# Performance work log

Hardware: AMD Instinct MI355X
Metric: run time of the kernel (lower is better)

## Reference

```python
import jax, jax.numpy as jnp
import numpy as np

NUM_SEQS = 32
MAX_PREFILL = 512
TOTAL_TOKENS = NUM_SEQS * MAX_PREFILL  # 16384
D_MODEL = 4096
VOCAB = 50257


def setup_inputs() -> dict:
    key = jax.random.key(0)
    k1, k2, k3 = jax.random.split(key, 3)
    hidden_states = jax.random.normal(k1, (TOTAL_TOKENS, D_MODEL), dtype=jnp.float32)
    embd_weight = jax.random.normal(k2, (VOCAB, D_MODEL), dtype=jnp.float32) * 0.02
    # per-sequence prefill lengths in [1, MAX_PREFILL]; cumsum <= TOTAL_TOKENS
    prefill_lens = jax.random.randint(k3, (NUM_SEQS,), 1, MAX_PREFILL + 1, dtype=jnp.int32)
    return {"hidden_states": hidden_states, "embd_weight": embd_weight,
            "prefill_lens": prefill_lens}


def reference(hidden_states, embd_weight, prefill_lens):
    # last-token index of each sequence in the flattened token stream
    indices = jnp.cumsum(prefill_lens) - 1            # [num_seqs]
    last_h = hidden_states[indices]                   # [num_seqs, d_model]
    logits = jnp.matmul(last_h, embd_weight.T)        # [num_seqs, vocab]
    logprobs = jax.nn.log_softmax(logits.astype(jnp.float32), axis=-1)
    ids = jnp.argmax(logprobs, axis=-1)               # [num_seqs]
    return ids
```

## Files before the change

kernel.cpp:

```cpp
#include <hip/hip_runtime.h>
#include <hip/hip_bf16.h>

#define D_MODEL 4096
#define VOCAB 50257
#define NUM_SEQS 32
#define NT 1571

typedef __attribute__((ext_vector_type(8))) short bf16x8;
typedef __attribute__((ext_vector_type(16))) float f32x16;


__device__ __forceinline__ void cvt2(float f, short* hi, short* lo) {
  union { __hip_bfloat16 b; short s; } h, l;
  h.b = __float2bfloat16(f);
  float hf = __bfloat162float(h.b);
  l.b = __float2bfloat16(f - hf);
  *hi = h.s; *lo = l.s;
}

__global__ void k_prep(const int* __restrict__ lens, int* __restrict__ idx) {
  if (threadIdx.x == 0) {
    int run = 0;
    for (int s = 0; s < NUM_SEQS; ++s) { run += lens[s]; idx[s] = run - 1; }
  }
}

__global__ void k_gather(const float* __restrict__ hs, const int* __restrict__ idx,
                         short* __restrict__ hBh, short* __restrict__ hBl) {
  int g = blockIdx.x * 512 + threadIdx.x;
  int s = g >> 12, k = g & 4095;
  float v = hs[(size_t)idx[s] * D_MODEL + k];
  short hi, lo; cvt2(v, &hi, &lo);
  int off = ((k >> 3) * 32 + s) * 8 + (k & 7);
  hBh[off] = hi; hBl[off] = lo;
}

__global__ __launch_bounds__(64) void k_mfma(const float* __restrict__ W,
    const short* __restrict__ hBh, const short* __restrict__ hBl,
    unsigned long long* __restrict__ wbest) {
  const int lane = threadIdx.x;
  const int half = lane >> 5;
  const int r32 = lane & 31;
  const int tile = blockIdx.x;
  const int wrow = min(tile * 32 + r32, VOCAB - 1);
  const float* wp = W + (size_t)wrow * D_MODEL + half * 8;
  const short* bph = hBh + ((size_t)half * 32 + r32) * 8;
  const short* bpl = hBl + ((size_t)half * 32 + r32) * 8;

  f32x16 accA, accB;
#pragma unroll
  for (int i = 0; i < 16; ++i) { accA[i] = 0.f; accB[i] = 0.f; }

  float4 a0 = *(const float4*)(wp);
  float4 a1 = *(const float4*)(wp + 4);
  float4 p0 = *(const float4*)(wp + 16);
  float4 p1 = *(const float4*)(wp + 20);
  bf16x8 bh = *(const bf16x8*)(bph);
  bf16x8 bl = *(const bf16x8*)(bpl);

#pragma unroll 1
  for (int t = 0; t < 256; ++t) {
    const int t2 = (t + 2 < 256) ? t + 2 : 0;
    const int t1 = (t + 1 < 256) ? t + 1 : 0;
    float4 n0 = *(const float4*)(wp + 16 * t2);
    float4 n1 = *(const float4*)(wp + 16 * t2 + 4);
    bf16x8 nbh = *(const bf16x8*)(bph + 512 * t1);
    bf16x8 nbl = *(const bf16x8*)(bpl + 512 * t1);

    float fa[8] = {a0.x, a0.y, a0.z, a0.w, a1.x, a1.y, a1.z, a1.w};
    bf16x8 ahi, alo;
#pragma unroll
    for (int e = 0; e < 8; ++e) {
      short hi, lo; cvt2(fa[e], &hi, &lo);
      ahi[e] = hi; alo[e] = lo;
    }

    accA = __builtin_amdgcn_mfma_f32_32x32x16_bf16(ahi, bh, accA, 0, 0, 0);
    accB = __builtin_amdgcn_mfma_f32_32x32x16_bf16(ahi, bl, accB, 0, 0, 0);
    accA = __builtin_amdgcn_mfma_f32_32x32x16_bf16(alo, bh, accA, 0, 0, 0);

    a0 = p0; a1 = p1; p0 = n0; p1 = n1; bh = nbh; bl = nbl;
  }

#pragma unroll
  for (int i = 0; i < 16; ++i) accA[i] += accB[i];

  unsigned long long best = 0ull;
#pragma unroll
  for (int r = 0; r < 16; ++r) {
    int row = (r & 3) + 8 * (r >> 2) + 4 * half;
    int v = tile * 32 + row;
    if (v < VOCAB) {
      unsigned u = __float_as_uint(accA[r]);
      u = (u & 0x80000000u) ? ~u : (u | 0x80000000u);
      unsigned long long key = ((unsigned long long)u << 32) | (unsigned)(~v);
      if (key > best) best = key;
    }
  }
  unsigned long long o = __shfl_xor(best, 32, 64);
  if (o > best) best = o;
  if (half == 0) wbest[(size_t)tile * 32 + r32] = best;
}

__global__ __launch_bounds__(256) void k_final(
    const unsigned long long* __restrict__ wbest, int* __restrict__ out) {
  int s = blockIdx.x;
  unsigned long long best = 0ull;
  for (int i = threadIdx.x; i < NT; i += 256) {
    unsigned long long k = wbest[(size_t)i * 32 + s];
    if (k > best) best = k;
  }
#pragma unroll
  for (int off = 32; off > 0; off >>= 1) {
    unsigned long long o = __shfl_xor(best, off, 64);
    if (o > best) best = o;
  }
  __shared__ unsigned long long lred[4];
  if ((threadIdx.x & 63) == 0) lred[threadIdx.x >> 6] = best;
  __syncthreads();
  if (threadIdx.x == 0) {
#pragma unroll
    for (int i = 1; i < 4; ++i) if (lred[i] > best) best = lred[i];
    out[s] = (int)(~(unsigned)(best & 0xFFFFFFFFull));
  }
}

extern "C" void kernel_launch(void* const* d_in, const int* in_sizes, int n_in,
                              void* d_out, int out_size, void* d_ws, size_t ws_size,
                              hipStream_t stream) {
  const float* hs  = (const float*)d_in[0];
  const float* W   = (const float*)d_in[1];
  const int* lens  = (const int*)d_in[2];

  char* ws = (char*)d_ws;
  int* idx = (int*)ws;
  short* hBh = (short*)(ws + 4096);
  short* hBl = (short*)(ws + 266240);
  unsigned long long* wbest = (unsigned long long*)(ws + 528384);
  int* out = (int*)d_out;

  k_prep<<<1, 64, 0, stream>>>(lens, idx);
  k_gather<<<256, 512, 0, stream>>>(hs, idx, hBh, hBl);
  k_mfma<<<NT, 64, 0, stream>>>(W, hBh, hBl, wbest);
  k_final<<<NUM_SEQS, 256, 0, stream>>>(wbest, out);
}
```

Baseline: 204.5 us.

## Split K across two waves per tile, deepen prefetch, reduce argmax via atomicMax

Each 32-row vocab tile is now processed by two waves, each covering half of the K dimension, and their partial accumulators are combined through shared memory. The W prefetch depth goes from two to three steps. Per-tile best keys are merged with a 64-bit atomicMax into a 32-entry global array instead of a per-tile buffer and a reduction kernel, leaving k_final as a trivial decode. This raises memory-level parallelism for streaming the fp32 weight matrix, at the cost of an LDS exchange, a barrier and atomic contention on 32 addresses.

```diff
diff --git a/kernel.cpp b/kernel.cpp
--- a/kernel.cpp
+++ b/kernel.cpp
@@ -5,6 +5,8 @@
 #define VOCAB 50257
 #define NUM_SEQS 32
 #define NT 1571
+#define KW 2048
+#define TSTEPS (KW / 16)
 
 typedef __attribute__((ext_vector_type(8))) short bf16x8;
 typedef __attribute__((ext_vector_type(16))) float f32x16;
@@ -18,11 +20,14 @@
   *hi = h.s; *lo = l.s;
 }
 
-__global__ void k_prep(const int* __restrict__ lens, int* __restrict__ idx) {
-  if (threadIdx.x == 0) {
+__global__ void k_prep(const int* __restrict__ lens, int* __restrict__ idx,
+                       unsigned long long* __restrict__ gkeys) {
+  int t = threadIdx.x;
+  if (t == 0) {
     int run = 0;
     for (int s = 0; s < NUM_SEQS; ++s) { run += lens[s]; idx[s] = run - 1; }
   }
+  if (t < NUM_SEQS) gkeys[t] = 0ull;
 }
 
 __global__ void k_gather(const float* __restrict__ hs, const int* __restrict__ idx,
@@ -35,35 +40,35 @@
   hBh[off] = hi; hBl[off] = lo;
 }
 
-__global__ __launch_bounds__(64) void k_mfma(const float* __restrict__ W,
+__global__ __launch_bounds__(128) void k_mfma(const float* __restrict__ W,
     const short* __restrict__ hBh, const short* __restrict__ hBl,
-    unsigned long long* __restrict__ wbest) {
-  const int lane = threadIdx.x;
+    unsigned long long* __restrict__ gkeys) {
+  const int lane = threadIdx.x & 63;
+  const int wv = threadIdx.x >> 6;
   const int half = lane >> 5;
   const int r32 = lane & 31;
   const int tile = blockIdx.x;
   const int wrow = min(tile * 32 + r32, VOCAB - 1);
-  const float* wp = W + (size_t)wrow * D_MODEL + half * 8;
-  const short* bph = hBh + ((size_t)half * 32 + r32) * 8;
-  const short* bpl = hBl + ((size_t)half * 32 + r32) * 8;
+  const int k0 = wv * KW;
+  const float4* wr = (const float4*)(W + (size_t)wrow * D_MODEL + k0 + half * 8);
+  const short* bph = hBh + (((size_t)(k0 >> 3) + half) * 32 + r32) * 8;
+  const short* bpl = hBl + (((size_t)(k0 >> 3) + half) * 32 + r32) * 8;
 
   f32x16 accA, accB;
 #pragma unroll
   for (int i = 0; i < 16; ++i) { accA[i] = 0.f; accB[i] = 0.f; }
 
-  float4 a0 = *(const float4*)(wp);
-  float4 a1 = *(const float4*)(wp + 4);
-  float4 p0 = *(const float4*)(wp + 16);
-  float4 p1 = *(const float4*)(wp + 20);
+  float4 a0 = wr[0], a1 = wr[1];
+  float4 b0 = wr[4], b1 = wr[5];
+  float4 c0 = wr[8], c1 = wr[9];
   bf16x8 bh = *(const bf16x8*)(bph);
   bf16x8 bl = *(const bf16x8*)(bpl);
 
 #pragma unroll 1
-  for (int t = 0; t < 256; ++t) {
-    const int t2 = (t + 2 < 256) ? t + 2 : 0;
-    const int t1 = (t + 1 < 256) ? t + 1 : 0;
-    float4 n0 = *(const float4*)(wp + 16 * t2);
-    float4 n1 = *(const float4*)(wp + 16 * t2 + 4);
+  for (int t = 0; t < TSTEPS; ++t) {
+    const int t3 = (t + 3 < TSTEPS) ? t + 3 : 0;
+    const int t1 = (t + 1 < TSTEPS) ? t + 1 : 0;
+    float4 d0 = wr[4 * t3], d1 = wr[4 * t3 + 1];
     bf16x8 nbh = *(const bf16x8*)(bph + 512 * t1);
     bf16x8 nbl = *(const bf16x8*)(bpl + 512 * t1);
 
@@ -79,50 +84,46 @@
     accB = __builtin_amdgcn_mfma_f32_32x32x16_bf16(ahi, bl, accB, 0, 0, 0);
     accA = __builtin_amdgcn_mfma_f32_32x32x16_bf16(alo, bh, accA, 0, 0, 0);
 
-    a0 = p0; a1 = p1; p0 = n0; p1 = n1; bh = nbh; bl = nbl;
+    a0 = b0; a1 = b1; b0 = c0; b1 = c1; c0 = d0; c1 = d1;
+    bh = nbh; bl = nbl;
   }
 
 #pragma unroll
   for (int i = 0; i < 16; ++i) accA[i] += accB[i];
 
-  unsigned long long best = 0ull;
+  __shared__ float red[64][17];
+  if (wv == 1) {
 #pragma unroll
-  for (int r = 0; r < 16; ++r) {
-    int row = (r & 3) + 8 * (r >> 2) + 4 * half;
-    int v = tile * 32 + row;
-    if (v < VOCAB) {
-      unsigned u = __float_as_uint(accA[r]);
-      u = (u & 0x80000000u) ? ~u : (u | 0x80000000u);
-      unsigned long long key = ((unsigned long long)u << 32) | (unsigned)(~v);
-      if (key > best) best = key;
+    for (int i = 0; i < 16; ++i) red[lane][i] = accA[i];
+  }
+  __syncthreads();
+  if (wv == 0) {
+#pragma unroll
+    for (int i = 0; i < 16; ++i) accA[i] += red[lane][i];
+
+    unsigned long long best = 0ull;
+#pragma unroll
+    for (int r = 0; r < 16; ++r) {
+      int row = (r & 3) + 8 * (r >> 2) + 4 * half;
+      int v = tile * 32 + row;
+      if (v < VOCAB) {
+        unsigned u = __float_as_uint(accA[r]);
+        u = (u & 0x80000000u) ? ~u : (u | 0x80000000u);
+        unsigned long long key = ((unsigned long long)u << 32) | (unsigned)(~v);
+        if (key > best) best = key;
+      }
     }
+    unsigned long long o = __shfl_xor(best, 32, 64);
+    if (o > best) best = o;
+    if (half == 0) atomicMax(&gkeys[r32], best);
   }
-  unsigned long long o = __shfl_xor(best, 32, 64);
-  if (o > best) best = o;
-  if (half == 0) wbest[(size_t)tile * 32 + r32] = best;
 }
 
-__global__ __launch_bounds__(256) void k_final(
-    const unsigned long long* __restrict__ wbest, int* __restrict__ out) {
-  int s = blockIdx.x;
-  unsigned long long best = 0ull;
-  for (int i = threadIdx.x; i < NT; i += 256) {
-    unsigned long long k = wbest[(size_t)i * 32 + s];
-    if (k > best) best = k;
-  }
-#pragma unroll
-  for (int off = 32; off > 0; off >>= 1) {
-    unsigned long long o = __shfl_xor(best, off, 64);
-    if (o > best) best = o;
-  }
-  __shared__ unsigned long long lred[4];
-  if ((threadIdx.x & 63) == 0) lred[threadIdx.x >> 6] = best;
-  __syncthreads();
-  if (threadIdx.x == 0) {
-#pragma unroll
-    for (int i = 1; i < 4; ++i) if (lred[i] > best) best = lred[i];
-    out[s] = (int)(~(unsigned)(best & 0xFFFFFFFFull));
-  }
+__global__ void k_final(const unsigned long long* __restrict__ gkeys,
+                        int* __restrict__ out) {
+  int s = threadIdx.x;
+  if (s < NUM_SEQS)
+    out[s] = (int)(~(unsigned)(gkeys[s] & 0xFFFFFFFFull));
 }
 
 extern "C" void kernel_launch(void* const* d_in, const int* in_sizes, int n_in,
@@ -134,13 +135,13 @@
 
   char* ws = (char*)d_ws;
   int* idx = (int*)ws;
+  unsigned long long* gkeys = (unsigned long long*)(ws + 512);
   short* hBh = (short*)(ws + 4096);
   short* hBl = (short*)(ws + 266240);
-  unsigned long long* wbest = (unsigned long long*)(ws + 528384);
   int* out = (int*)d_out;
 
-  k_prep<<<1, 64, 0, stream>>>(lens, idx);
+  k_prep<<<1, 64, 0, stream>>>(lens, idx, gkeys);
   k_gather<<<256, 512, 0, stream>>>(hs, idx, hBh, hBl);
-  k_mfma<<<NT, 64, 0, stream>>>(W, hBh, hBl, wbest);
-  k_final<<<NUM_SEQS, 256, 0, stream>>>(wbest, out);
+  k_mfma<<<NT, 128, 0, stream>>>(W, hBh, hBl, gkeys);
+  k_final<<<1, 64, 0, stream>>>(gkeys, out);
 }
```

After: 260.4 us. 27.3% more time.

## Split the K dimension of the logits GEMM across four blocks with a reduction kernel

Applied to the files above, without the earlier changes.

The MFMA kernel now launches a 2D grid that splits the 4096-wide reduction into four slices. Each block writes partial 32x32 logits to a workspace buffer, and a new reduce kernel sums the slices and performs the per-tile argmax. The goal is more blocks in flight: 1571 single-wave blocks underfill the GPU, and each wave had a long serial K loop for streaming the fp32 weight matrix. The cost is an extra kernel launch and about 25 MB of partial-sum traffic written and then read back.

```diff
diff --git a/kernel.cpp b/kernel.cpp
--- a/kernel.cpp
+++ b/kernel.cpp
@@ -5,6 +5,9 @@
 #define VOCAB 50257
 #define NUM_SEQS 32
 #define NT 1571
+#define KSP 4
+#define KW (D_MODEL / KSP)
+#define TSTEPS (KW / 16)
 
 typedef __attribute__((ext_vector_type(8))) short bf16x8;
 typedef __attribute__((ext_vector_type(16))) float f32x16;
@@ -37,15 +40,17 @@
 
 __global__ __launch_bounds__(64) void k_mfma(const float* __restrict__ W,
     const short* __restrict__ hBh, const short* __restrict__ hBl,
-    unsigned long long* __restrict__ wbest) {
+    float* __restrict__ part) {
   const int lane = threadIdx.x;
   const int half = lane >> 5;
   const int r32 = lane & 31;
   const int tile = blockIdx.x;
+  const int kq = blockIdx.y;
+  const int k0 = kq * KW;
   const int wrow = min(tile * 32 + r32, VOCAB - 1);
-  const float* wp = W + (size_t)wrow * D_MODEL + half * 8;
-  const short* bph = hBh + ((size_t)half * 32 + r32) * 8;
-  const short* bpl = hBl + ((size_t)half * 32 + r32) * 8;
+  const float* wp = W + (size_t)wrow * D_MODEL + k0 + half * 8;
+  const short* bph = hBh + (((size_t)(k0 >> 3) + half) * 32 + r32) * 8;
+  const short* bpl = hBl + (((size_t)(k0 >> 3) + half) * 32 + r32) * 8;
 
   f32x16 accA, accB;
 #pragma unroll
@@ -59,9 +64,9 @@
   bf16x8 bl = *(const bf16x8*)(bpl);
 
 #pragma unroll 1
-  for (int t = 0; t < 256; ++t) {
-    const int t2 = (t + 2 < 256) ? t + 2 : 0;
-    const int t1 = (t + 1 < 256) ? t + 1 : 0;
+  for (int t = 0; t < TSTEPS; ++t) {
+    const int t2 = (t + 2 < TSTEPS) ? t + 2 : 0;
+    const int t1 = (t + 1 < TSTEPS) ? t + 1 : 0;
     float4 n0 = *(const float4*)(wp + 16 * t2);
     float4 n1 = *(const float4*)(wp + 16 * t2 + 4);
     bf16x8 nbh = *(const bf16x8*)(bph + 512 * t1);
@@ -82,16 +87,33 @@
     a0 = p0; a1 = p1; p0 = n0; p1 = n1; bh = nbh; bl = nbl;
   }
 
+  float* pc = part + ((size_t)kq * NT + tile) * 1024;
 #pragma unroll
-  for (int i = 0; i < 16; ++i) accA[i] += accB[i];
+  for (int r = 0; r < 16; ++r) {
+    int row = (r & 3) + 8 * (r >> 2) + 4 * half;
+    pc[row * 32 + r32] = accA[r] + accB[r];
+  }
+}
+
+__global__ __launch_bounds__(64) void k_reduce(const float* __restrict__ part,
+                                               unsigned long long* __restrict__ wbest) {
+  const int tile = blockIdx.x;
+  const int l = threadIdx.x;
+  const int s = l & 31;
+  const int rbase = (l >> 5) * 16;
+  const float* p0 = part + (size_t)tile * 1024;
 
   unsigned long long best = 0ull;
 #pragma unroll
   for (int r = 0; r < 16; ++r) {
-    int row = (r & 3) + 8 * (r >> 2) + 4 * half;
-    int v = tile * 32 + row;
+    const int row = rbase + r;
+    const int v = tile * 32 + row;
+    float x = 0.f;
+#pragma unroll
+    for (int q = 0; q < KSP; ++q)
+      x += p0[(size_t)q * NT * 1024 + row * 32 + s];
     if (v < VOCAB) {
-      unsigned u = __float_as_uint(accA[r]);
+      unsigned u = __float_as_uint(x);
       u = (u & 0x80000000u) ? ~u : (u | 0x80000000u);
       unsigned long long key = ((unsigned long long)u << 32) | (unsigned)(~v);
       if (key > best) best = key;
@@ -99,7 +121,7 @@
   }
   unsigned long long o = __shfl_xor(best, 32, 64);
   if (o > best) best = o;
-  if (half == 0) wbest[(size_t)tile * 32 + r32] = best;
+  if (l < 32) wbest[(size_t)tile * 32 + s] = best;
 }
 
 __global__ __launch_bounds__(256) void k_final(
@@ -137,10 +159,13 @@
   short* hBh = (short*)(ws + 4096);
   short* hBl = (short*)(ws + 266240);
   unsigned long long* wbest = (unsigned long long*)(ws + 528384);
+  float* part = (float*)(ws + (1 << 20));
   int* out = (int*)d_out;
 
   k_prep<<<1, 64, 0, stream>>>(lens, idx);
   k_gather<<<256, 512, 0, stream>>>(hs, idx, hBh, hBl);
-  k_mfma<<<NT, 64, 0, stream>>>(W, hBh, hBl, wbest);
+  dim3 grid(NT, KSP);
+  k_mfma<<<grid, 64, 0, stream>>>(W, hBh, hBl, part);
+  k_reduce<<<NT, 64, 0, stream>>>(part, wbest);
   k_final<<<NUM_SEQS, 256, 0, stream>>>(wbest, out);
 }
```

Result: slower. 255.9 us (+25.1%).

## Stage weight tiles through double-buffered LDS with coalesced loads and split-K across waves

Applied to the files above, without the earlier changes.

Each block now has four waves. They load the 32-row weight tile in 256-column chunks as fully coalesced float4 rows, stage them in double-buffered padded LDS, and split the K range of each chunk so each wave handles a quarter. Partial accumulators are combined through shared memory before the argmax. The aim is to replace the strided per-lane row reads of the original single-wave kernel with coalesced streaming, and to hide latency with more waves. In exchange it adds a barrier per chunk, uses a lot of LDS, which limits occupancy, and adds a final cross-wave reduction.

```diff
diff --git a/kernel.cpp b/kernel.cpp
--- a/kernel.cpp
+++ b/kernel.cpp
@@ -5,6 +5,9 @@
 #define VOCAB 50257
 #define NUM_SEQS 32
 #define NT 1571
+#define BK 256
+#define NCH (D_MODEL / BK)
+#define SROW 260
 
 typedef __attribute__((ext_vector_type(8))) short bf16x8;
 typedef __attribute__((ext_vector_type(16))) float f32x16;
@@ -35,15 +38,27 @@
   hBh[off] = hi; hBl[off] = lo;
 }
 
-__global__ __launch_bounds__(64) void k_mfma(const float* __restrict__ W,
+__global__ __launch_bounds__(256, 2) void k_mfma(const float* __restrict__ W,
     const short* __restrict__ hBh, const short* __restrict__ hBl,
     unsigned long long* __restrict__ wbest) {
-  const int lane = threadIdx.x;
+  __shared__ float lds[2][32 * SROW];
+  __shared__ float comb[3][64][17];
+
+  const int tid = threadIdx.x;
+  const int lane = tid & 63;
+  const int wv = tid >> 6;
   const int half = lane >> 5;
   const int r32 = lane & 31;
   const int tile = blockIdx.x;
-  const int wrow = min(tile * 32 + r32, VOCAB - 1);
-  const float* wp = W + (size_t)wrow * D_MODEL + half * 8;
+
+  const int scol = tid & 63;
+  const float* bases[8];
+#pragma unroll
+  for (int p = 0; p < 8; ++p) {
+    int wr = min(tile * 32 + p * 4 + wv, VOCAB - 1);
+    bases[p] = W + (size_t)wr * D_MODEL + scol * 4;
+  }
+
   const short* bph = hBh + ((size_t)half * 32 + r32) * 8;
   const short* bpl = hBl + ((size_t)half * 32 + r32) * 8;
 
@@ -51,55 +66,86 @@
 #pragma unroll
   for (int i = 0; i < 16; ++i) { accA[i] = 0.f; accB[i] = 0.f; }
 
-  float4 a0 = *(const float4*)(wp);
-  float4 a1 = *(const float4*)(wp + 4);
-  float4 p0 = *(const float4*)(wp + 16);
-  float4 p1 = *(const float4*)(wp + 20);
-  bf16x8 bh = *(const bf16x8*)(bph);
-  bf16x8 bl = *(const bf16x8*)(bpl);
+  float4 streg[8];
+#pragma unroll
+  for (int p = 0; p < 8; ++p) streg[p] = *(const float4*)(bases[p]);
+#pragma unroll
+  for (int p = 0; p < 8; ++p)
+    *(float4*)&lds[0][(p * 4 + wv) * SROW + scol * 4] = streg[p];
+  __syncthreads();
 
+  bf16x8 bh = *(const bf16x8*)(bph + 512 * (wv * 4));
+  bf16x8 bl = *(const bf16x8*)(bpl + 512 * (wv * 4));
+
+  int buf = 0;
 #pragma unroll 1
-  for (int t = 0; t < 256; ++t) {
-    const int t2 = (t + 2 < 256) ? t + 2 : 0;
-    const int t1 = (t + 1 < 256) ? t + 1 : 0;
-    float4 n0 = *(const float4*)(wp + 16 * t2);
-    float4 n1 = *(const float4*)(wp + 16 * t2 + 4);
-    bf16x8 nbh = *(const bf16x8*)(bph + 512 * t1);
-    bf16x8 nbl = *(const bf16x8*)(bpl + 512 * t1);
+  for (int c = 0; c < NCH; ++c) {
+    if (c + 1 < NCH) {
+#pragma unroll
+      for (int p = 0; p < 8; ++p)
+        streg[p] = *(const float4*)(bases[p] + (c + 1) * BK);
+    }
+#pragma unroll
+    for (int j = 0; j < 4; ++j) {
+      int tn = (j < 3) ? (c * 16 + wv * 4 + j + 1)
+                       : ((c + 1 < NCH) ? ((c + 1) * 16 + wv * 4) : 0);
+      bf16x8 nbh = *(const bf16x8*)(bph + 512 * tn);
+      bf16x8 nbl = *(const bf16x8*)(bpl + 512 * tn);
+      const float* ap = &lds[buf][r32 * SROW + wv * 64 + j * 16 + half * 8];
+      float4 a0 = *(const float4*)(ap);
+      float4 a1 = *(const float4*)(ap + 4);
 
-    float fa[8] = {a0.x, a0.y, a0.z, a0.w, a1.x, a1.y, a1.z, a1.w};
-    bf16x8 ahi, alo;
+      float fa[8] = {a0.x, a0.y, a0.z, a0.w, a1.x, a1.y, a1.z, a1.w};
+      bf16x8 ahi, alo;
 #pragma unroll
-    for (int e = 0; e < 8; ++e) {
-      short hi, lo; cvt2(fa[e], &hi, &lo);
-      ahi[e] = hi; alo[e] = lo;
+      for (int e = 0; e < 8; ++e) {
+        short hi, lo; cvt2(fa[e], &hi, &lo);
+        ahi[e] = hi; alo[e] = lo;
+      }
+      accA = __builtin_amdgcn_mfma_f32_32x32x16_bf16(ahi, bh, accA, 0, 0, 0);
+      accB = __builtin_amdgcn_mfma_f32_32x32x16_bf16(ahi, bl, accB, 0, 0, 0);
+      accA = __builtin_amdgcn_mfma_f32_32x32x16_bf16(alo, bh, accA, 0, 0, 0);
+      bh = nbh; bl = nbl;
     }
-
-    accA = __builtin_amdgcn_mfma_f32_32x32x16_bf16(ahi, bh, accA, 0, 0, 0);
-    accB = __builtin_amdgcn_mfma_f32_32x32x16_bf16(ahi, bl, accB, 0, 0, 0);
-    accA = __builtin_amdgcn_mfma_f32_32x32x16_bf16(alo, bh, accA, 0, 0, 0);
-
-    a0 = p0; a1 = p1; p0 = n0; p1 = n1; bh = nbh; bl = nbl;
+    if (c + 1 < NCH) {
+#pragma unroll
+      for (int p = 0; p < 8; ++p)
+        *(float4*)&lds[buf ^ 1][(p * 4 + wv) * SROW + scol * 4] = streg[p];
+    }
+    __syncthreads();
+    buf ^= 1;
   }
 
 #pragma unroll
   for (int i = 0; i < 16; ++i) accA[i] += accB[i];
 
-  unsigned long long best = 0ull;
+  if (wv > 0) {
 #pragma unroll
-  for (int r = 0; r < 16; ++r) {
-    int row = (r & 3) + 8 * (r >> 2) + 4 * half;
-    int v = tile * 32 + row;
-    if (v < VOCAB) {
-      unsigned u = __float_as_uint(accA[r]);
-      u = (u & 0x80000000u) ? ~u : (u | 0x80000000u);
-      unsigned long long key = ((unsigned long long)u << 32) | (unsigned)(~v);
-      if (key > best) best = key;
+    for (int i = 0; i < 16; ++i) comb[wv - 1][lane][i] = accA[i];
+  }
+  __syncthreads();
+  if (wv == 0) {
+#pragma unroll
+    for (int w = 0; w < 3; ++w)
+#pragma unroll
+      for (int i = 0; i < 16; ++i) accA[i] += comb[w][lane][i];
+
+    unsigned long long best = 0ull;
+#pragma unroll
+    for (int r = 0; r < 16; ++r) {
+      int row = (r & 3) + 8 * (r >> 2) + 4 * half;
+      int v = tile * 32 + row;
+      if (v < VOCAB) {
+        unsigned u = __float_as_uint(accA[r]);
+        u = (u & 0x80000000u) ? ~u : (u | 0x80000000u);
+        unsigned long long key = ((unsigned long long)u << 32) | (unsigned)(~v);
+        if (key > best) best = key;
+      }
     }
+    unsigned long long o = __shfl_xor(best, 32, 64);
+    if (o > best) best = o;
+    if (half == 0) wbest[(size_t)tile * 32 + r32] = best;
   }
-  unsigned long long o = __shfl_xor(best, 32, 64);
-  if (o > best) best = o;
-  if (half == 0) wbest[(size_t)tile * 32 + r32] = best;
 }
 
 __global__ __launch_bounds__(256) void k_final(
@@ -141,6 +187,6 @@
 
   k_prep<<<1, 64, 0, stream>>>(lens, idx);
   k_gather<<<256, 512, 0, stream>>>(hs, idx, hBh, hBl);
-  k_mfma<<<NT, 64, 0, stream>>>(W, hBh, hBl, wbest);
+  k_mfma<<<NT, 256, 0, stream>>>(W, hBh, hBl, wbest);
   k_final<<<NUM_SEQS, 256, 0, stream>>>(wbest, out);
 }
```

Result: slower. 359.0 us (+75.5%).
